# Performance work log

Hardware: AMD Instinct MI355X
Metric: run time of the kernel (lower is better)

The kernel has to match this reference:

```python
import jax, jax.numpy as jnp
import numpy as np

EPS = 1e-5  # BatchNorm1d default eps
NUM_HEADS = 8


def repbn(x, alpha, gamma, beta, rm, rv):
    # eval-mode RepBN over the channel (last) dim: BN(running stats) + alpha * x
    bn = (x - rm) * (gamma / jnp.sqrt(rv + EPS)) + beta
    return bn + alpha * x


def _forward(x, W_qkv, b_qkv, W_proj, b_proj, W1, b1, W2, b2, sa_w, sa_b,
             alpha1, gamma1, beta1, rm1, rv1, alpha2, gamma2, beta2, rm2, rv2):
    B, C, H, W = x.shape
    N = H * W
    D = C // NUM_HEADS
    t = x.reshape(B, C, N).transpose(0, 2, 1)  # [B, N, C]
    # --- FlashAttention (manual MHSA) ---
    qkv = (t @ W_qkv + b_qkv).reshape(B, N, 3, NUM_HEADS, D)
    q = qkv[:, :, 0].transpose(0, 2, 1, 3)  # [B, h, N, D]
    k = qkv[:, :, 1].transpose(0, 2, 1, 3)
    v = qkv[:, :, 2].transpose(0, 2, 1, 3)
    attn = jax.nn.softmax(jnp.einsum('bhnd,bhmd->bhnm', q, k) * (D ** -0.5), axis=-1)
    o = jnp.einsum('bhnm,bhmd->bhnd', attn, v).transpose(0, 2, 1, 3).reshape(B, N, C)
    o = o @ W_proj + b_proj
    # residual + blended norm (eval -> RepBN)
    t = repbn(t + o, alpha1, gamma1, beta1, rm1, rv1)
    # --- FFN with SpatialSILU activation ---
    h = t @ W1 + b1  # [B, N, cm]
    # depthwise 1x1 conv over the batch dim (channels==B per original unsqueeze(0))
    wgt = sa_w[:, None, None] * h + sa_b[:, None, None]
    h = h * jax.nn.sigmoid(wgt * h)
    f = h @ W2 + b2
    t = repbn(t + f, alpha2, gamma2, beta2, rm2, rv2)
    return t.transpose(0, 2, 1).reshape(B, C, H, W)


def setup_inputs() -> dict:
    key = jax.random.key(0)
    ks = jax.random.split(key, 8)
    B, C, H, W = 256, 256, 14, 14
    cm = 2048
    s = 0.02
    f32 = jnp.float32
    return {
        'x': jax.random.normal(ks[0], (B, C, H, W), f32),
        'W_qkv': jax.random.normal(ks[1], (C, 3 * C), f32) * s,
        'b_qkv': jnp.zeros((3 * C,), f32),
        'W_proj': jax.random.normal(ks[2], (C, C), f32) * s,
        'b_proj': jnp.zeros((C,), f32),
        'W1': jax.random.normal(ks[3], (C, cm), f32) * s,
        'b1': jnp.zeros((cm,), f32),
        'W2': jax.random.normal(ks[4], (cm, C), f32) * s,
        'b2': jnp.zeros((C,), f32),
        'sa_w': jax.random.normal(ks[5], (B,), f32) * s,
        'sa_b': jnp.zeros((B,), f32),
        'alpha1': jnp.ones((), f32),
        'gamma1': jnp.ones((C,), f32),
        'beta1': jnp.zeros((C,), f32),
        'rm1': jax.random.normal(ks[6], (C,), f32) * 0.1,
        'rv1': jnp.ones((C,), f32),
        'alpha2': jnp.ones((), f32),
        'gamma2': jnp.ones((C,), f32),
        'beta2': jnp.zeros((C,), f32),
        'rm2': jax.random.normal(ks[7], (C,), f32) * 0.1,
        'rv2': jnp.ones((C,), f32),
    }


def reference(x, W_qkv, b_qkv, W_proj, b_proj, W1, b1, W2, b2, sa_w, sa_b,
              alpha1, gamma1, beta1, rm1, rv1, alpha2, gamma2, beta2, rm2, rv2):
    return _forward(x, W_qkv, b_qkv, W_proj, b_proj, W1, b1, W2, b2, sa_w, sa_b,
                    alpha1, gamma1, beta1, rm1, rv1, alpha2, gamma2, beta2, rm2, rv2)
```

## Files before the change

### kernel.cpp

```cpp
#include <hip/hip_runtime.h>

using u16 = unsigned short;

typedef __bf16 bf16x8 __attribute__((ext_vector_type(8)));
typedef u16    u16x8  __attribute__((ext_vector_type(8)));
typedef float  f32x4  __attribute__((ext_vector_type(4)));

__device__ __forceinline__ float b2f(u16 u) {
    union { unsigned int i; float f; } c; c.i = ((unsigned int)u) << 16; return c.f;
}
__device__ __forceinline__ u16 f2b(float f) {
    union { float f; unsigned int i; } c; c.f = f;
    unsigned int i = c.i;
    return (u16)((i + 0x7FFFu + ((i >> 16) & 1u)) >> 16);
}
__device__ __forceinline__ unsigned cvtpk(float lo, float hi) {
    unsigned d;
    asm("v_cvt_pk_bf16_f32 %0, %1, %2" : "=v"(d) : "v"(lo), "v"(hi));
    return d;
}

#define AS1 __attribute__((address_space(1)))
#define AS3 __attribute__((address_space(3)))
__device__ __forceinline__ void glds16(const u16* g, u16* l) {
    __builtin_amdgcn_global_load_lds((const AS1 void*)(const void*)g,
                                     (AS3 void*)(void*)l, 16, 0, 0);
}

__global__ void btrans_f2b(const float* __restrict__ in, u16* __restrict__ out, int R, int C) {
    __shared__ u16 tile[32][33];
    const int c0 = blockIdx.x * 32, r0 = blockIdx.y * 32;
    const size_t base = (size_t)blockIdx.z * R * C;
    const int tx = threadIdx.x, ty = threadIdx.y;
    #pragma unroll
    for (int i = ty; i < 32; i += 8) {
        int r = r0 + i, c = c0 + tx;
        tile[i][tx] = (r < R && c < C) ? f2b(in[base + (size_t)r * C + c]) : (u16)0;
    }
    __syncthreads();
    #pragma unroll
    for (int i = ty; i < 32; i += 8) {
        int c = c0 + i, r = r0 + tx;
        if (c < C && r < R) out[base + (size_t)c * R + r] = tile[tx][i];
    }
}

__global__ void btrans_b2f(const u16* __restrict__ in, float* __restrict__ out, int R, int C) {
    __shared__ u16 tile[32][33];
    const int c0 = blockIdx.x * 32, r0 = blockIdx.y * 32;
    const size_t base = (size_t)blockIdx.z * R * C;
    const int tx = threadIdx.x, ty = threadIdx.y;
    #pragma unroll
    for (int i = ty; i < 32; i += 8) {
        int r = r0 + i, c = c0 + tx;
        tile[i][tx] = (r < R && c < C) ? in[base + (size_t)r * C + c] : (u16)0;
    }
    __syncthreads();
    #pragma unroll
    for (int i = ty; i < 32; i += 8) {
        int c = c0 + i, r = r0 + tx;
        if (c < C && r < R) out[base + (size_t)c * R + r] = b2f(tile[tx][i]);
    }
}

template<int EPI>
__launch_bounds__(512, 4)
__global__ void gemm_bt(const u16* __restrict__ A, const u16* __restrict__ BT,
                        const float* __restrict__ bias, u16* __restrict__ C,
                        int M, int N, int K, int row0,
                        const u16* __restrict__ R0,
                        const float* __restrict__ g, const float* __restrict__ be,
                        const float* __restrict__ rmv, const float* __restrict__ rvv,
                        const float* __restrict__ alpha,
                        const float* __restrict__ saw, const float* __restrict__ sab) {
    __shared__ __align__(16) u16 SL[24576];
    const int tid  = threadIdx.x;
    const int wave = tid >> 6, lane = tid & 63;
    const int wm = wave >> 1, wn = wave & 1;
    const int quad = lane >> 4, l16 = lane & 15;

    const unsigned gx = gridDim.x;
    unsigned lin = blockIdx.y * gx + blockIdx.x;
    const unsigned nwg = gx * gridDim.y;
    const unsigned q8 = nwg >> 3, r8 = nwg & 7;
    const unsigned xcd = lin & 7, loc = lin >> 3;
    lin = (xcd < r8 ? xcd * (q8 + 1) : r8 * (q8 + 1) + (xcd - r8) * q8) + loc;
    const int m0 = (int)(lin / gx) * 256, n0 = (int)(lin % gx) * 128;

    const int srow = lane >> 2;
    const int scol = (((lane & 3) ^ ((srow >> 1) & 3)) * 8);
    const size_t aoff0 = (size_t)(m0 + wave * 32 + srow) * K + scol;
    const size_t aoff1 = aoff0 + (size_t)16 * K;
    const size_t boff  = (size_t)(n0 + wave * 16 + srow) * K + scol;

    const int cfrag = (quad ^ ((l16 >> 1) & 3)) * 8;

    f32x4 acc[4][4] = {};
    const int niter = K >> 5;

    auto stage = [&](int buf, size_t kn) {
        glds16(A  + aoff0 + kn, SL + buf * 8192 + wave * 1024);
        glds16(A  + aoff1 + kn, SL + buf * 8192 + wave * 1024 + 512);
        glds16(BT + boff  + kn, SL + 16384 + buf * 4096 + wave * 512);
    };

    auto kstep = [&](int cur, int kt) {
        __syncthreads();
        if (kt + 1 < niter) stage(cur ^ 1, (size_t)(kt + 1) << 5);
        const u16* ab = SL + cur * 8192;
        const u16* bb = SL + 16384 + cur * 4096;
        bf16x8 af[4], bfr[4];
        #pragma unroll
        for (int i = 0; i < 4; i++)
            af[i] = *(const bf16x8*)&ab[(wm * 64 + i * 16 + l16) * 32 + cfrag];
        #pragma unroll
        for (int j = 0; j < 4; j++)
            bfr[j] = *(const bf16x8*)&bb[(wn * 64 + j * 16 + l16) * 32 + cfrag];
        #pragma unroll
        for (int i = 0; i < 4; i++)
            #pragma unroll
            for (int j = 0; j < 4; j++)
                acc[i][j] = __builtin_amdgcn_mfma_f32_16x16x32_bf16(af[i], bfr[j], acc[i][j], 0, 0, 0);
    };

    stage(0, 0);
    int kt = 0;
    for (; kt + 2 <= niter; kt += 2) { kstep(0, kt); kstep(1, kt + 1); }
    if (kt < niter) kstep(kt & 1, kt);

    __syncthreads();

    float alphav = 0.f;
    if (EPI == 1) alphav = alpha[0];

    float biasv[4], k0v[4], k1v[4];
    #pragma unroll
    for (int j = 0; j < 4; j++) {
        const int col = n0 + wn * 64 + j * 16 + l16;
        biasv[j] = bias[col];
        if (EPI == 1) {
            float sc = g[col] * rsqrtf(rvv[col] + 1e-5f);
            k1v[j] = sc + alphav;
            k0v[j] = be[col] - rmv[col] * sc;
        }
    }

    const int dup = l16 & 1;
    const int pr  = l16 >> 1;
    u16* Crow = C + (size_t)(m0 + wm * 64 + quad * 4 + 2 * dup) * N
                  + (n0 + wn * 64 + pr * 2);

    auto emit = [&]() {
        #pragma unroll
        for (int i = 0; i < 4; i++) {
            float swv4[4], sbv4[4];
            if (EPI == 2) {
                #pragma unroll
                for (int r = 0; r < 4; r++) {
                    const int row = row0 + m0 + wm * 64 + i * 16 + quad * 4 + r;
                    const int bidx = row / 196;
                    swv4[r] = saw[bidx]; sbv4[r] = sab[bidx];
                }
            }
            #pragma unroll
            for (int j = 0; j < 4; j++) {
                float vv[4];
                #pragma unroll
                for (int r = 0; r < 4; r++) {
                    float v = acc[i][j][r] + biasv[j];
                    if (EPI == 1) {
                        const int rowL = (wm & 1) * 64 + i * 16 + quad * 4 + r;
                        const int colp = wn * 64 + j * 16 + (l16 & ~1);
                        unsigned rd = *(const unsigned*)&SL[rowL * 128 + colp];
                        unsigned fb = dup ? (rd & 0xffff0000u) : (rd << 16);
                        union { unsigned u; float f; } cc; cc.u = fb;
                        float x = v + cc.f;
                        v = fmaf(x, k1v[j], k0v[j]);
                    } else if (EPI == 2) {
                        float w = fmaf(swv4[r], v, sbv4[r]);
                        v = v / (1.f + __expf(-w * v));
                    }
                    vv[r] = v;
                }
                unsigned D[4];
                #pragma unroll
                for (int r = 0; r < 4; r++) {
                    float o  = __shfl_xor(vv[r], 1, 64);
                    float lo = dup ? o : vv[r];
                    float hi = dup ? vv[r] : o;
                    D[r] = cvtpk(lo, hi);
                }
                unsigned s0 = dup ? D[2] : D[0];
                unsigned s1 = dup ? D[3] : D[1];
                u16* p = Crow + (size_t)i * 16 * N + j * 16;
                *(unsigned*)p       = s0;
                *(unsigned*)(p + N) = s1;
            }
        }
    };

    if (EPI == 1) {
        #pragma unroll
        for (int h = 0; h < 2; h++) {
            for (int c = tid; c < 2048; c += 512) {
                int row = c >> 4, colc = (c & 15) * 8;
                *(u16x8*)&SL[row * 128 + colc] =
                    *(const u16x8*)&R0[(size_t)(m0 + h * 128 + row) * N + n0 + colc];
            }
            __syncthreads();
            if ((wm >> 1) == h) emit();
            __syncthreads();
        }
    } else {
        emit();
    }
}

__launch_bounds__(256)
__global__ void attn_kernel(const u16* __restrict__ qkv, u16* __restrict__ o) {
    __shared__ __align__(16) u16 Kb[224 * 32];
    __shared__ __align__(16) u16 Vt[32 * 232];
    __shared__ __align__(16) u16 Pl[4][16 * 232];
    const int tid  = threadIdx.x;
    const int wave = tid >> 6, lane = tid & 63;
    const int quad = lane >> 4, l16 = lane & 15;
    const int b = blockIdx.x >> 3, h = blockIdx.x & 7;
    const u16* qg = qkv + (size_t)b * 196 * 768 + h * 32;
    const float scale = 0.17677669529663687f;

    for (int idx = tid; idx < 896; idx += 256) {
        int row = idx >> 2, dp = (idx & 3) * 8;
        u16x8 kv = {};
        if (row < 196) kv = *(const u16x8*)&qg[(size_t)row * 768 + 256 + dp];
        *(u16x8*)&Kb[row * 32 + dp] = kv;
    }
    for (int idx = tid; idx < 896; idx += 256) {
        int row = idx >> 2, dp = (idx & 3) * 8;
        u16x8 vv = {};
        if (row < 196) vv = *(const u16x8*)&qg[(size_t)row * 768 + 512 + dp];
        #pragma unroll
        for (int e = 0; e < 8; e++) Vt[(dp + e) * 232 + row] = vv[e];
    }
    for (int c = lane; c < 16 * 24; c += 64) {
        int m = c / 24, cc = 208 + (c % 24);
        Pl[wave][m * 232 + cc] = 0;
    }
    __syncthreads();

    for (int t = wave; t < 13; t += 4) {
        const int m0 = t * 16;
        bf16x8 aq = {};
        const int qrow = m0 + l16;
        if (qrow < 196) aq = *(const bf16x8*)&qg[(size_t)qrow * 768 + quad * 8];

        f32x4 s[13];
        #pragma unroll
        for (int ct = 0; ct < 13; ct++) {
            bf16x8 bk = *(const bf16x8*)&Kb[(ct * 16 + l16) * 32 + quad * 8];
            s[ct] = __builtin_amdgcn_mfma_f32_16x16x32_bf16(aq, bk, (f32x4){0.f, 0.f, 0.f, 0.f}, 0, 0, 0);
        }
        if (l16 >= 4) {
            #pragma unroll
            for (int r = 0; r < 4; r++) s[12][r] = -1e30f;
        }
        float mx[4] = {-1e30f, -1e30f, -1e30f, -1e30f};
        #pragma unroll
        for (int ct = 0; ct < 13; ct++)
            #pragma unroll
            for (int r = 0; r < 4; r++) mx[r] = fmaxf(mx[r], s[ct][r]);
        #pragma unroll
        for (int off = 1; off < 16; off <<= 1)
            #pragma unroll
            for (int r = 0; r < 4; r++) mx[r] = fmaxf(mx[r], __shfl_xor(mx[r], off, 64));
        float sum[4] = {0.f, 0.f, 0.f, 0.f};
        #pragma unroll
        for (int ct = 0; ct < 13; ct++) {
            #pragma unroll
            for (int r = 0; r < 4; r++) {
                float p = __expf((s[ct][r] - mx[r]) * scale);
                sum[r] += p;
                Pl[wave][(quad * 4 + r) * 232 + ct * 16 + l16] = f2b(p);
            }
        }
        #pragma unroll
        for (int off = 1; off < 16; off <<= 1)
            #pragma unroll
            for (int r = 0; r < 4; r++) sum[r] += __shfl_xor(sum[r], off, 64);
        float inv[4];
        #pragma unroll
        for (int r = 0; r < 4; r++) inv[r] = 1.f / sum[r];

        #pragma unroll
        for (int nt = 0; nt < 2; nt++) {
            f32x4 ao = {0.f, 0.f, 0.f, 0.f};
            #pragma unroll
            for (int kc = 0; kc < 7; kc++) {
                bf16x8 ap = *(const bf16x8*)&Pl[wave][l16 * 232 + kc * 32 + quad * 8];
                bf16x8 bv = *(const bf16x8*)&Vt[(nt * 16 + l16) * 232 + kc * 32 + quad * 8];
                ao = __builtin_amdgcn_mfma_f32_16x16x32_bf16(ap, bv, ao, 0, 0, 0);
            }
            #pragma unroll
            for (int r = 0; r < 4; r++) {
                const int gm = m0 + quad * 4 + r;
                if (gm < 196)
                    o[((size_t)b * 196 + gm) * 256 + h * 32 + nt * 16 + l16] = f2b(ao[r] * inv[r]);
            }
        }
    }
}

extern "C" void kernel_launch(void* const* d_in, const int* in_sizes, int n_in,
                              void* d_out, int out_size, void* d_ws, size_t ws_size,
                              hipStream_t stream) {
    const float* x      = (const float*)d_in[0];
    const float* Wqkv   = (const float*)d_in[1];
    const float* bqkv   = (const float*)d_in[2];
    const float* Wproj  = (const float*)d_in[3];
    const float* bproj  = (const float*)d_in[4];
    const float* W1     = (const float*)d_in[5];
    const float* b1     = (const float*)d_in[6];
    const float* W2     = (const float*)d_in[7];
    const float* b2     = (const float*)d_in[8];
    const float* saw    = (const float*)d_in[9];
    const float* sab    = (const float*)d_in[10];
    const float* alpha1 = (const float*)d_in[11];
    const float* g1     = (const float*)d_in[12];
    const float* be1    = (const float*)d_in[13];
    const float* rm1    = (const float*)d_in[14];
    const float* rv1    = (const float*)d_in[15];
    const float* alpha2 = (const float*)d_in[16];
    const float* g2     = (const float*)d_in[17];
    const float* be2    = (const float*)d_in[18];
    const float* rm2    = (const float*)d_in[19];
    const float* rv2    = (const float*)d_in[20];

    const int B = 256, Cc = 256, Np = 196, CM = 2048;
    const int M = B * Np;

    auto al = [](size_t s) { return (s + 255) & ~(size_t)255; };
    char* ws = (char*)d_ws;
    const size_t o_t0  = 0;
    const size_t o_t1  = o_t0 + al((size_t)M * Cc * 2);
    const size_t o_wq  = o_t1 + al((size_t)M * Cc * 2);
    const size_t o_wp  = o_wq + al((size_t)768 * Cc * 2);
    const size_t o_w1  = o_wp + al((size_t)Cc * Cc * 2);
    const size_t o_w2  = o_w1 + al((size_t)Cc * CM * 2);
    const size_t o_scr = o_w2 + al((size_t)CM * Cc * 2);
    const size_t S = (ws_size > o_scr) ? ws_size - o_scr : 0;

    u16* t0     = (u16*)(ws + o_t0);
    u16* t1b    = (u16*)(ws + o_t1);
    u16* WqkvT  = (u16*)(ws + o_wq);
    u16* WprojT = (u16*)(ws + o_wp);
    u16* W1T    = (u16*)(ws + o_w1);
    u16* W2T    = (u16*)(ws + o_w2);
    u16* scr    = (u16*)(ws + o_scr);
    u16* t2     = t0;
    u16* obuf   = (u16*)d_out;
    float* out  = (float*)d_out;

    int nq = 1; while (nq < 4 && ((size_t)(M / nq) * 768 * 2) > S) nq *= 2;
    const int nf_opts[6] = {1, 2, 4, 14, 28, 56};
    int nf = 56;
    for (int i = 0; i < 6; ++i) {
        if (((size_t)(M / nf_opts[i]) * CM * 2) <= S) { nf = nf_opts[i]; break; }
    }
    const int Mq = M / nq, Bq = B / nq;
    const int Mf = M / nf;

    dim3 tb(32, 8, 1);
    btrans_f2b<<<dim3((Np + 31) / 32, (Cc + 31) / 32, B), tb, 0, stream>>>(x, t0, Cc, Np);
    btrans_f2b<<<dim3(768 / 32, Cc / 32, 1), tb, 0, stream>>>(Wqkv,  WqkvT,  Cc, 768);
    btrans_f2b<<<dim3(Cc  / 32, Cc / 32, 1), tb, 0, stream>>>(Wproj, WprojT, Cc, Cc);
    btrans_f2b<<<dim3(CM  / 32, Cc / 32, 1), tb, 0, stream>>>(W1,    W1T,    Cc, CM);
    btrans_f2b<<<dim3(Cc  / 32, CM / 32, 1), tb, 0, stream>>>(W2,    W2T,    CM, Cc);

    for (int c = 0; c < nq; ++c) {
        gemm_bt<0><<<dim3(768 / 128, Mq / 256), 512, 0, stream>>>(
            t0 + (size_t)c * Mq * Cc, WqkvT, bqkv, scr, Mq, 768, Cc, 0,
            nullptr, nullptr, nullptr, nullptr, nullptr, nullptr, nullptr, nullptr);
        attn_kernel<<<dim3(Bq * 8), 256, 0, stream>>>(scr, obuf + (size_t)c * Mq * Cc);
    }

    gemm_bt<1><<<dim3(Cc / 128, M / 256), 512, 0, stream>>>(
        obuf, WprojT, bproj, t1b, M, Cc, Cc, 0,
        t0, g1, be1, rm1, rv1, alpha1, nullptr, nullptr);

    for (int c = 0; c < nf; ++c) {
        gemm_bt<2><<<dim3(CM / 128, Mf / 256), 512, 0, stream>>>(
            t1b + (size_t)c * Mf * Cc, W1T, b1, scr, Mf, CM, Cc, c * Mf,
            nullptr, nullptr, nullptr, nullptr, nullptr, nullptr, saw, sab);
        gemm_bt<1><<<dim3(Cc / 128, Mf / 256), 512, 0, stream>>>(
            scr, W2T, b2, t2 + (size_t)c * Mf * Cc, Mf, Cc, CM, 0,
            t1b + (size_t)c * Mf * Cc, g2, be2, rm2, rv2, alpha2, nullptr, nullptr);
    }

    btrans_b2f<<<dim3((Cc + 31) / 32, (Np + 31) / 32, B), tb, 0, stream>>>(t2, out, Np, Cc);
}
```

Baseline: 517.0 us.

## Add K-resident A-tile GEMM for K=256 projections with pre-tiled weights

Adds a new GEMM kernel for the K=256 GEMMs (QKV, output projection, FFN up-projection). Each 64-row block of A is loaded once into LDS and stays there while the kernel sweeps all N columns. The weight matrices are pre-tiled into the MFMA fragment layout, so each wave reads B fragments straight from global memory into registers without LDS staging. The aim is to avoid re-reading A once per column tile and to cut LDS traffic and sync overhead. The cost is per-sweep global B loads with no reuse across waves, and a fixed K of 256 hardcoded into the kernel.

Result: slower. 1.081 ms (+109.2%).

```diff
diff --git a/kernel.cpp b/kernel.cpp
--- a/kernel.cpp
+++ b/kernel.cpp
@@ -60,6 +60,146 @@
     for (int i = ty; i < 32; i += 8) {
         int c = c0 + i, r = r0 + tx;
         if (c < C && r < R) out[base + (size_t)c * R + r] = b2f(tile[tx][i]);
+    }
+}
+
+__global__ void wtile_f2b(const float* __restrict__ in, u16* __restrict__ out, int N) {
+    const int lane = threadIdx.x;
+    const int colblk = blockIdx.x, kt = blockIdx.y;
+    const int l16 = lane & 15, quad = lane >> 4;
+    const int col = colblk * 16 + l16;
+    u16x8 tmp;
+    #pragma unroll
+    for (int e = 0; e < 8; e++) {
+        const int k = kt * 32 + quad * 8 + e;
+        tmp[e] = f2b(in[(size_t)k * N + col]);
+    }
+    *(u16x8*)&out[(size_t)colblk * 4096 + kt * 512 + l16 * 32 + quad * 8] = tmp;
+}
+
+template<int EPI>
+__launch_bounds__(256, 3)
+__global__ void gemm_kres(const u16* __restrict__ A, const u16* __restrict__ BT,
+                          const float* __restrict__ bias, u16* __restrict__ C,
+                          int N, int row0,
+                          const u16* __restrict__ R0,
+                          const float* __restrict__ g, const float* __restrict__ be,
+                          const float* __restrict__ rmv, const float* __restrict__ rvv,
+                          const float* __restrict__ alpha,
+                          const float* __restrict__ saw, const float* __restrict__ sab) {
+    __shared__ __align__(16) u16 AL[8][2048];
+    const int tid = threadIdx.x, wave = tid >> 6, lane = tid & 63;
+    const int quad = lane >> 4, l16 = lane & 15;
+    const int m0 = blockIdx.x * 64;
+
+    {
+        const int srow = lane >> 2;
+        const int scol = (((lane & 3) ^ ((srow >> 1) & 3)) * 8);
+        #pragma unroll
+        for (int t = 0; t < 2; t++) {
+            const int kt = wave * 2 + t;
+            #pragma unroll
+            for (int rb = 0; rb < 4; rb++) {
+                glds16(A + (size_t)(m0 + rb * 16 + srow) * 256 + kt * 32 + scol,
+                       &AL[kt][rb * 512]);
+            }
+        }
+    }
+    __syncthreads();
+
+    const int cfrag = (quad ^ ((l16 >> 1) & 3)) * 8;
+    const int dup = l16 & 1, pr = l16 >> 1;
+    const float alphav = (EPI == 1) ? alpha[0] : 0.f;
+
+    float s0w = 0.f, s0b = 0.f, s1w = 0.f, s1b = 0.f; int rowB = 0x7fffffff;
+    if (EPI == 2) {
+        const int bidx0 = (row0 + m0) / 196;
+        const int bi1 = (bidx0 + 1 < 256) ? bidx0 + 1 : 255;
+        rowB = (bidx0 + 1) * 196;
+        s0w = saw[bidx0]; s0b = sab[bidx0];
+        s1w = saw[bi1];   s1b = sab[bi1];
+    }
+
+    const int nsweep = N >> 7;
+    for (int s = 0; s < nsweep; s++) {
+        const int c0 = s * 128 + wave * 32;
+
+        bf16x8 bfr[2][8];
+        const u16* bbase = BT + (size_t)(c0 >> 4) * 4096 + l16 * 32 + quad * 8;
+        #pragma unroll
+        for (int j = 0; j < 2; j++)
+            #pragma unroll
+            for (int kt = 0; kt < 8; kt++)
+                bfr[j][kt] = *(const bf16x8*)(bbase + j * 4096 + kt * 512);
+
+        float biasv[2];
+        biasv[0] = bias[c0 + l16];
+        biasv[1] = bias[c0 + 16 + l16];
+        float k0p[2][2], k1p[2][2];
+        if (EPI == 1) {
+            #pragma unroll
+            for (int j = 0; j < 2; j++)
+                #pragma unroll
+                for (int p = 0; p < 2; p++) {
+                    const int col = c0 + j * 16 + pr * 2 + p;
+                    const float sc = g[col] * rsqrtf(rvv[col] + 1e-5f);
+                    k1p[j][p] = sc + alphav;
+                    k0p[j][p] = be[col] - rmv[col] * sc;
+                }
+        }
+
+        f32x4 acc[4][2] = {};
+        #pragma unroll
+        for (int kt = 0; kt < 8; kt++) {
+            bf16x8 af[4];
+            #pragma unroll
+            for (int i = 0; i < 4; i++)
+                af[i] = *(const bf16x8*)&AL[kt][(i * 16 + l16) * 32 + cfrag];
+            #pragma unroll
+            for (int i = 0; i < 4; i++) {
+                acc[i][0] = __builtin_amdgcn_mfma_f32_16x16x32_bf16(af[i], bfr[0][kt], acc[i][0], 0, 0, 0);
+                acc[i][1] = __builtin_amdgcn_mfma_f32_16x16x32_bf16(af[i], bfr[1][kt], acc[i][1], 0, 0, 0);
+            }
+        }
+
+        const int r0i = 2 * dup, r1i = r0i + 1;
+        #pragma unroll
+        for (int i = 0; i < 4; i++) {
+            #pragma unroll
+            for (int j = 0; j < 2; j++) {
+                float vv[4];
+                #pragma unroll
+                for (int r = 0; r < 4; r++) {
+                    float v = acc[i][j][r] + biasv[j];
+                    if (EPI == 2) {
+                        const int rg = row0 + m0 + i * 16 + quad * 4 + r;
+                        const bool hb = rg >= rowB;
+                        const float w = fmaf(hb ? s1w : s0w, v, hb ? s1b : s0b);
+                        v = v / (1.f + __expf(-w * v));
+                    }
+                    vv[r] = v;
+                }
+                float ot[4];
+                #pragma unroll
+                for (int r = 0; r < 4; r++) ot[r] = __shfl_xor(vv[r], 1, 64);
+                float lo0 = dup ? ot[r0i] : vv[r0i], hi0 = dup ? vv[r0i] : ot[r0i];
+                float lo1 = dup ? ot[r1i] : vv[r1i], hi1 = dup ? vv[r1i] : ot[r1i];
+                if (EPI == 1) {
+                    const u16* rp = R0 + (size_t)(m0 + i * 16 + quad * 4 + r0i) * N
+                                       + (c0 + j * 16 + pr * 2);
+                    const unsigned rd0 = *(const unsigned*)rp;
+                    const unsigned rd1 = *(const unsigned*)(rp + N);
+                    lo0 = fmaf(lo0 + b2f((u16)(rd0 & 0xffff)), k1p[j][0], k0p[j][0]);
+                    hi0 = fmaf(hi0 + b2f((u16)(rd0 >> 16)),    k1p[j][1], k0p[j][1]);
+                    lo1 = fmaf(lo1 + b2f((u16)(rd1 & 0xffff)), k1p[j][0], k0p[j][0]);
+                    hi1 = fmaf(hi1 + b2f((u16)(rd1 >> 16)),    k1p[j][1], k0p[j][1]);
+                }
+                u16* p = C + (size_t)(m0 + i * 16 + quad * 4 + 2 * dup) * N
+                           + (c0 + j * 16 + pr * 2);
+                *(unsigned*)p       = cvtpk(lo0, hi0);
+                *(unsigned*)(p + N) = cvtpk(lo1, hi1);
+            }
+        }
     }
 }
 
@@ -370,25 +510,25 @@
 
     dim3 tb(32, 8, 1);
     btrans_f2b<<<dim3((Np + 31) / 32, (Cc + 31) / 32, B), tb, 0, stream>>>(x, t0, Cc, Np);
-    btrans_f2b<<<dim3(768 / 32, Cc / 32, 1), tb, 0, stream>>>(Wqkv,  WqkvT,  Cc, 768);
-    btrans_f2b<<<dim3(Cc  / 32, Cc / 32, 1), tb, 0, stream>>>(Wproj, WprojT, Cc, Cc);
-    btrans_f2b<<<dim3(CM  / 32, Cc / 32, 1), tb, 0, stream>>>(W1,    W1T,    Cc, CM);
-    btrans_f2b<<<dim3(Cc  / 32, CM / 32, 1), tb, 0, stream>>>(W2,    W2T,    CM, Cc);
+    wtile_f2b<<<dim3(768 / 16, 8), 64, 0, stream>>>(Wqkv,  WqkvT,  768);
+    wtile_f2b<<<dim3(Cc  / 16, 8), 64, 0, stream>>>(Wproj, WprojT, Cc);
+    wtile_f2b<<<dim3(CM  / 16, 8), 64, 0, stream>>>(W1,    W1T,    CM);
+    btrans_f2b<<<dim3(Cc / 32, CM / 32, 1), tb, 0, stream>>>(W2, W2T, CM, Cc);
 
     for (int c = 0; c < nq; ++c) {
-        gemm_bt<0><<<dim3(768 / 128, Mq / 256), 512, 0, stream>>>(
-            t0 + (size_t)c * Mq * Cc, WqkvT, bqkv, scr, Mq, 768, Cc, 0,
+        gemm_kres<0><<<dim3(Mq / 64), 256, 0, stream>>>(
+            t0 + (size_t)c * Mq * Cc, WqkvT, bqkv, scr, 768, 0,
             nullptr, nullptr, nullptr, nullptr, nullptr, nullptr, nullptr, nullptr);
         attn_kernel<<<dim3(Bq * 8), 256, 0, stream>>>(scr, obuf + (size_t)c * Mq * Cc);
     }
 
-    gemm_bt<1><<<dim3(Cc / 128, M / 256), 512, 0, stream>>>(
-        obuf, WprojT, bproj, t1b, M, Cc, Cc, 0,
+    gemm_kres<1><<<dim3(M / 64), 256, 0, stream>>>(
+        obuf, WprojT, bproj, t1b, Cc, 0,
         t0, g1, be1, rm1, rv1, alpha1, nullptr, nullptr);
 
     for (int c = 0; c < nf; ++c) {
-        gemm_bt<2><<<dim3(CM / 128, Mf / 256), 512, 0, stream>>>(
-            t1b + (size_t)c * Mf * Cc, W1T, b1, scr, Mf, CM, Cc, c * Mf,
+        gemm_kres<2><<<dim3(Mf / 64), 256, 0, stream>>>(
+            t1b + (size_t)c * Mf * Cc, W1T, b1, scr, CM, c * Mf,
             nullptr, nullptr, nullptr, nullptr, nullptr, nullptr, saw, sab);
         gemm_bt<1><<<dim3(Cc / 128, Mf / 256), 512, 0, stream>>>(
             scr, W2T, b2, t2 + (size_t)c * Mf * Cc, Mf, Cc, CM, 0,
```

## Add 256x256-tile 8-wave GEMM with XCD remap for the FFN GEMMs

Applied to the files above, without the earlier changes.

Adds a new GEMM kernel that uses 256x256 output tiles, 8 waves, and a 64-wide K step with double-buffered LDS (128KB). It interleaves direct global-to-LDS loads with MFMA sub-blocks, uses setprio around the MFMA clusters, and remaps workgroup ids across XCDs. The two FFN GEMMs now use this kernel in place of the 256x128 one, and the smallest chunk option (56) is dropped so each FFN chunk spans at least 256 rows. Larger tiles raise operand reuse and arithmetic intensity. The cost is lower occupancy and fewer workgroups per launch; the second FFN GEMM gets only one column block per row tile.

New measurement: 650.2 us. 25.8% more time.

```diff
diff --git a/kernel.cpp b/kernel.cpp
--- a/kernel.cpp
+++ b/kernel.cpp
@@ -60,6 +60,169 @@
     for (int i = ty; i < 32; i += 8) {
         int c = c0 + i, r = r0 + tx;
         if (c < C && r < R) out[base + (size_t)c * R + r] = b2f(tile[tx][i]);
+    }
+}
+
+#define MM8(MS,NS) do{ \
+    __builtin_amdgcn_s_barrier(); \
+    asm volatile("s_waitcnt lgkmcnt(0)" ::: "memory"); \
+    __builtin_amdgcn_sched_barrier(0); \
+    __builtin_amdgcn_s_setprio(1); \
+    _Pragma("unroll") \
+    for (int f = 0; f < 4; f++) { \
+      acc[(MS)*4+f][(NS)*2+0] = __builtin_amdgcn_mfma_f32_16x16x32_bf16(af[f][0], bf[0][0], acc[(MS)*4+f][(NS)*2+0],0,0,0); \
+      acc[(MS)*4+f][(NS)*2+0] = __builtin_amdgcn_mfma_f32_16x16x32_bf16(af[f][1], bf[0][1], acc[(MS)*4+f][(NS)*2+0],0,0,0); \
+      acc[(MS)*4+f][(NS)*2+1] = __builtin_amdgcn_mfma_f32_16x16x32_bf16(af[f][0], bf[1][0], acc[(MS)*4+f][(NS)*2+1],0,0,0); \
+      acc[(MS)*4+f][(NS)*2+1] = __builtin_amdgcn_mfma_f32_16x16x32_bf16(af[f][1], bf[1][1], acc[(MS)*4+f][(NS)*2+1],0,0,0); \
+    } \
+    __builtin_amdgcn_s_setprio(0); \
+    __builtin_amdgcn_sched_barrier(0); \
+    __builtin_amdgcn_s_barrier(); \
+}while(0)
+
+template<int EPI>
+__launch_bounds__(512, 2)
+__global__ void gemm8(const u16* __restrict__ A, const u16* __restrict__ BT,
+                      const float* __restrict__ bias, u16* __restrict__ C,
+                      int N, int K, int row0,
+                      const u16* __restrict__ R0,
+                      const float* __restrict__ g, const float* __restrict__ be,
+                      const float* __restrict__ rmv, const float* __restrict__ rvv,
+                      const float* __restrict__ alpha,
+                      const float* __restrict__ saw, const float* __restrict__ sab) {
+    __shared__ __align__(16) u16 SL[65536];
+    const int tid = threadIdx.x, wave = tid >> 6, lane = tid & 63;
+    const int wm = wave >> 2, wn = wave & 3;
+    const int quad = lane >> 4, l16 = lane & 15;
+
+    const unsigned gx = gridDim.x;
+    unsigned lin = blockIdx.y * gx + blockIdx.x;
+    const unsigned nwg = gx * gridDim.y;
+    const unsigned q8 = nwg >> 3, r8 = nwg & 7;
+    const unsigned xcd = lin & 7, loc = lin >> 3;
+    lin = (xcd < r8 ? xcd * (q8 + 1) : r8 * (q8 + 1) + (xcd - r8) * q8) + loc;
+    const int m0 = (int)(lin / gx) * 256, n0 = (int)(lin % gx) * 256;
+
+    const int T = K >> 6;
+
+    const int srow = lane >> 2;
+    const int scol = (((lane & 3) ^ ((srow >> 1) & 3)) * 8);
+    const int ci0 = wave * 2;
+
+    auto issueHalf = [&](int mat, int h, int t) {
+        const u16* src = (mat == 0) ? (A + (size_t)(m0 + h * 128) * K)
+                                    : (BT + (size_t)(n0 + h * 128) * K);
+        u16* dst = SL + mat * 32768 + (t & 1) * 16384 + h * 8192;
+        #pragma unroll
+        for (int i = 0; i < 2; i++) {
+            const int ci = ci0 + i, rg = ci >> 1, kc = ci & 1;
+            glds16(src + (size_t)(rg * 16 + srow) * K + t * 64 + kc * 32 + scol,
+                   dst + kc * 4096 + rg * 512);
+        }
+    };
+
+    const int cfrag = (quad ^ ((l16 >> 1) & 3)) * 8;
+    f32x4 acc[8][4] = {};
+    bf16x8 af[4][2], bf[2][2];
+
+    issueHalf(0, 0, 0); issueHalf(0, 1, 0); issueHalf(1, 0, 0); issueHalf(1, 1, 0);
+    if (T > 1) { issueHalf(0, 0, 1); asm volatile("s_waitcnt vmcnt(2)" ::: "memory"); }
+    else       {                     asm volatile("s_waitcnt vmcnt(0)" ::: "memory"); }
+    __builtin_amdgcn_s_barrier();
+
+    for (int t = 0; t < T; ++t) {
+        const int c = t & 1;
+        const bool nx = (t + 1 < T);
+        const u16* Ab = SL + c * 16384 + wm * 8192;
+        const u16* Bb = SL + 32768 + c * 16384 + (wn >> 1) * 8192;
+        const int bcol = (wn & 1) * 64;
+
+        auto rdAf = [&](int ms) {
+            #pragma unroll
+            for (int f = 0; f < 4; f++)
+                #pragma unroll
+                for (int kk = 0; kk < 2; kk++)
+                    af[f][kk] = *(const bf16x8*)&Ab[kk * 4096 + (ms * 64 + f * 16 + l16) * 32 + cfrag];
+        };
+        auto rdBf = [&](int ns) {
+            #pragma unroll
+            for (int gg = 0; gg < 2; gg++)
+                #pragma unroll
+                for (int kk = 0; kk < 2; kk++)
+                    bf[gg][kk] = *(const bf16x8*)&Bb[kk * 4096 + (bcol + ns * 32 + gg * 16 + l16) * 32 + cfrag];
+        };
+
+        rdAf(0); rdBf(0); if (nx) issueHalf(0, 1, t + 1); MM8(0, 0);
+        rdBf(1);          if (nx) issueHalf(1, 0, t + 1); MM8(0, 1);
+        rdAf(1);          if (nx) issueHalf(1, 1, t + 1); MM8(1, 1);
+        rdBf(0);                                          MM8(1, 0);
+
+        if (nx) {
+            if (t + 2 < T) { issueHalf(0, 0, t + 2); asm volatile("s_waitcnt vmcnt(2)" ::: "memory"); }
+            else           {                         asm volatile("s_waitcnt vmcnt(0)" ::: "memory"); }
+            __builtin_amdgcn_s_barrier();
+        }
+    }
+
+    const int dup = l16 & 1, pr = l16 >> 1;
+    const float alphav = (EPI == 1) ? alpha[0] : 0.f;
+    float biasv[4], k0p[4][2], k1p[4][2];
+    #pragma unroll
+    for (int j = 0; j < 4; j++) {
+        biasv[j] = bias[n0 + wn * 64 + j * 16 + l16];
+        if (EPI == 1) {
+            #pragma unroll
+            for (int p = 0; p < 2; p++) {
+                const int col = n0 + wn * 64 + j * 16 + pr * 2 + p;
+                const float sc = g[col] * rsqrtf(rvv[col] + 1e-5f);
+                k1p[j][p] = sc + alphav;
+                k0p[j][p] = be[col] - rmv[col] * sc;
+            }
+        }
+    }
+    const int r0i = 2 * dup, r1i = r0i + 1;
+
+    #pragma unroll
+    for (int i = 0; i < 8; i++) {
+        const int rowb = m0 + wm * 128 + i * 16 + quad * 4;
+        float swv4[4], sbv4[4];
+        if (EPI == 2) {
+            #pragma unroll
+            for (int r = 0; r < 4; r++) {
+                const int bidx = (row0 + rowb + r) / 196;
+                swv4[r] = saw[bidx]; sbv4[r] = sab[bidx];
+            }
+        }
+        #pragma unroll
+        for (int j = 0; j < 4; j++) {
+            float vv[4];
+            #pragma unroll
+            for (int r = 0; r < 4; r++) {
+                float v = acc[i][j][r] + biasv[j];
+                if (EPI == 2) {
+                    const float w = fmaf(swv4[r], v, sbv4[r]);
+                    v = v / (1.f + __expf(-w * v));
+                }
+                vv[r] = v;
+            }
+            float ot[4];
+            #pragma unroll
+            for (int r = 0; r < 4; r++) ot[r] = __shfl_xor(vv[r], 1, 64);
+            float lo0 = dup ? ot[r0i] : vv[r0i], hi0 = dup ? vv[r0i] : ot[r0i];
+            float lo1 = dup ? ot[r1i] : vv[r1i], hi1 = dup ? vv[r1i] : ot[r1i];
+            if (EPI == 1) {
+                const u16* rp = R0 + (size_t)(rowb + r0i) * N + (n0 + wn * 64 + j * 16 + pr * 2);
+                const unsigned rd0 = *(const unsigned*)rp;
+                const unsigned rd1 = *(const unsigned*)(rp + N);
+                lo0 = fmaf(lo0 + b2f((u16)(rd0 & 0xffff)), k1p[j][0], k0p[j][0]);
+                hi0 = fmaf(hi0 + b2f((u16)(rd0 >> 16)),    k1p[j][1], k0p[j][1]);
+                lo1 = fmaf(lo1 + b2f((u16)(rd1 & 0xffff)), k1p[j][0], k0p[j][0]);
+                hi1 = fmaf(hi1 + b2f((u16)(rd1 >> 16)),    k1p[j][1], k0p[j][1]);
+            }
+            u16* p = C + (size_t)(rowb + 2 * dup) * N + (n0 + wn * 64 + j * 16 + pr * 2);
+            *(unsigned*)p       = cvtpk(lo0, hi0);
+            *(unsigned*)(p + N) = cvtpk(lo1, hi1);
+        }
     }
 }
 
@@ -360,9 +523,9 @@
     float* out  = (float*)d_out;
 
     int nq = 1; while (nq < 4 && ((size_t)(M / nq) * 768 * 2) > S) nq *= 2;
-    const int nf_opts[6] = {1, 2, 4, 14, 28, 56};
-    int nf = 56;
-    for (int i = 0; i < 6; ++i) {
+    const int nf_opts[5] = {1, 2, 4, 14, 28};
+    int nf = 28;
+    for (int i = 0; i < 5; ++i) {
         if (((size_t)(M / nf_opts[i]) * CM * 2) <= S) { nf = nf_opts[i]; break; }
     }
     const int Mq = M / nq, Bq = B / nq;
@@ -387,11 +550,11 @@
         t0, g1, be1, rm1, rv1, alpha1, nullptr, nullptr);
 
     for (int c = 0; c < nf; ++c) {
-        gemm_bt<2><<<dim3(CM / 128, Mf / 256), 512, 0, stream>>>(
-            t1b + (size_t)c * Mf * Cc, W1T, b1, scr, Mf, CM, Cc, c * Mf,
+        gemm8<2><<<dim3(CM / 256, Mf / 256), 512, 0, stream>>>(
+            t1b + (size_t)c * Mf * Cc, W1T, b1, scr, CM, Cc, c * Mf,
             nullptr, nullptr, nullptr, nullptr, nullptr, nullptr, saw, sab);
-        gemm_bt<1><<<dim3(Cc / 128, Mf / 256), 512, 0, stream>>>(
-            scr, W2T, b2, t2 + (size_t)c * Mf * Cc, Mf, Cc, CM, 0,
+        gemm8<1><<<dim3(Cc / 256, Mf / 256), 512, 0, stream>>>(
+            scr, W2T, b2, t2 + (size_t)c * Mf * Cc, Cc, CM, 0,
             t1b + (size_t)c * Mf * Cc, g2, be2, rm2, rv2, alpha2, nullptr, nullptr);
     }
 
```
